# Optimization experiments

Measured on AMD Instinct MI355X. Metric: run time of the kernel, lower is better.

## Reference

```python
import jax, jax.numpy as jnp
import numpy as np

B, A, N, FIN, H, HEADS, OUT = 32, 64, 121, 12, 128, 4, 256
NL = 2          # transformer encoder layers
LEVELS = 4      # complete ternary tree: N = (3**(LEVELS+1)-1)//2 = 121
EPS = 1e-5


def setup_inputs() -> dict:
    key = jax.random.key(0)
    ks = jax.random.split(key, 10)
    s = 0.02
    # adjacency: complete ternary tree, local node indices, rows [parent, child, branch]
    child = np.arange(1, N)
    parent = (child - 1) // 3
    branch = (child - 1) % 3
    adj = np.stack([parent, child, branch], -1).astype(np.int32)  # (N-1, 3)
    adjacency = jnp.asarray(np.broadcast_to(adj, (B, A, N - 1, 3)).copy())
    perm = jax.random.permutation(ks[0], N)  # torch.randperm(n_nodes) equivalent
    forest = jax.random.normal(ks[1], (B, A, N, FIN), jnp.float32)
    p = lambda k, shape: s * jax.random.normal(k, shape, jnp.float32)
    return dict(
        forest=forest, adjacency=adjacency, perm=perm,
        w_in=p(ks[2], (H, FIN)), b_in=jnp.zeros((H,), jnp.float32),
        qkv_w=p(ks[3], (NL, 3 * H, H)), qkv_b=jnp.zeros((NL, 3 * H), jnp.float32),
        proj_w=p(ks[4], (NL, H, H)), proj_b=jnp.zeros((NL, H), jnp.float32),
        ff1_w=p(ks[5], (NL, H, H)), ff1_b=jnp.zeros((NL, H), jnp.float32),
        ff2_w=p(ks[6], (NL, H, H)), ff2_b=jnp.zeros((NL, H), jnp.float32),
        ln1_g=jnp.ones((NL, H), jnp.float32), ln1_b=jnp.zeros((NL, H), jnp.float32),
        ln2_g=jnp.ones((NL, H), jnp.float32), ln2_b=jnp.zeros((NL, H), jnp.float32),
        w_out=p(ks[7], (OUT, N * H)), b_out=jnp.zeros((OUT,), jnp.float32),
        lnf_g=jnp.ones((OUT,), jnp.float32), lnf_b=jnp.zeros((OUT,), jnp.float32))


def _ln(x, g, b):
    m = x.mean(-1, keepdims=True)
    v = ((x - m) ** 2).mean(-1, keepdims=True)  # biased var, as torch LayerNorm
    return (x - m) * jax.lax.rsqrt(v + EPS) * g + b


def _tree_pe(adjacency):
    """Level-parallel tree positional encoding: pe[child] = pe[parent] with
    bit (depth*3 + branch) set to 1 (depth 0 = first level below root)."""
    parent = adjacency[..., 0]
    branch = adjacency[..., 2]
    pe = jnp.zeros((B, A, N, H), jnp.float32)
    for l in range(1, LEVELS + 1):
        s0 = (3 ** l - 1) // 2          # first node index at level l
        e0 = (3 ** (l + 1) - 1) // 2    # one past last node at level l
        pa = parent[..., s0 - 1:e0 - 1]             # (B, A, n_l) parent local idx
        br = branch[..., s0 - 1:e0 - 1]             # (B, A, n_l) branch 0/1/2
        ppe = jnp.take_along_axis(pe, pa[..., None], axis=2)  # gather parent PE
        bits = jax.nn.one_hot((l - 1) * 3 + br, H, dtype=jnp.float32)
        pe = pe.at[:, :, s0:e0, :].set(ppe + bits)
    return pe


def _mha(x, wqkv, bqkv, wo, bo):
    S = x.shape[0]
    hd = H // HEADS
    qkv = x @ wqkv.T + bqkv
    q, k, v = [t.reshape(S, N, HEADS, hd) for t in jnp.split(qkv, 3, axis=-1)]
    logits = jnp.einsum('bqhd,bkhd->bhqk', q, k) / float(np.sqrt(hd))
    o = jnp.einsum('bhqk,bkhd->bqhd', jax.nn.softmax(logits, -1), v)
    return o.reshape(S, N, H) @ wo.T + bo


def _forward(forest, adjacency, perm, w_in, b_in, qkv_w, qkv_b, proj_w, proj_b,
             ff1_w, ff1_b, ff2_w, ff2_b, ln1_g, ln1_b, ln2_g, ln2_b,
             w_out, b_out, lnf_g, lnf_b):
    x = forest @ w_in.T + b_in + _tree_pe(adjacency)        # (B, A, N, H)
    x = x.reshape(B * A, N, H)[:, perm]                      # token shuffle
    for i in range(NL):  # post-norm encoder layers, relu FFN, dropout=0
        x = _ln(x + _mha(x, qkv_w[i], qkv_b[i], proj_w[i], proj_b[i]), ln1_g[i], ln1_b[i])
        h = jnp.maximum(x @ ff1_w[i].T + ff1_b[i], 0.0)
        x = _ln(x + h @ ff2_w[i].T + ff2_b[i], ln2_g[i], ln2_b[i])
    y = x.reshape(B * A, N * H) @ w_out.T + b_out
    return _ln(y.reshape(B, A, OUT), lnf_g, lnf_b)


def reference(forest, adjacency, perm, w_in, b_in, qkv_w, qkv_b, proj_w, proj_b,
              ff1_w, ff1_b, ff2_w, ff2_b, ln1_g, ln1_b, ln2_g, ln2_b,
              w_out, b_out, lnf_g, lnf_b):
    return _forward(forest, adjacency, perm, w_in, b_in, qkv_w, qkv_b, proj_w, proj_b,
                    ff1_w, ff1_b, ff2_w, ff2_b, ln1_g, ln1_b, ln2_g, ln2_b,
                    w_out, b_out, lnf_g, lnf_b)
```

## Files before the change

kernel.cpp:

```cpp
#include <hip/hip_runtime.h>


typedef unsigned short u16;
typedef __attribute__((ext_vector_type(8))) short bf16x8;
typedef __attribute__((ext_vector_type(4))) float f32x4;
typedef __attribute__((ext_vector_type(4))) unsigned int u32x4;
typedef __attribute__((ext_vector_type(2))) unsigned int u32x2;

#define NTOK 121
#define HD 128
#define S_TOT 2048
#define EPSF 1e-5f

__device__ inline u16 f2bf(float f) {
  unsigned u = __float_as_uint(f);
  return (u16)((u + 0x7FFFu + ((u >> 16) & 1u)) >> 16);
}
__device__ inline float bf2f(u16 h) { return __uint_as_float(((unsigned)h) << 16); }
__device__ inline float bfu32lo(unsigned u) { return __uint_as_float(u << 16); }
__device__ inline float bfu32hi(unsigned u) { return __uint_as_float(u & 0xffff0000u); }

__device__ inline f32x4 mfma16(bf16x8 a, bf16x8 b, f32x4 c) {
  return __builtin_amdgcn_mfma_f32_16x16x32_bf16(a, b, c, 0, 0, 0);
}

__device__ inline unsigned cvt_pk_bf16(float lo, float hi) {
  unsigned r;
  asm("v_cvt_pk_bf16_f32 %0, %1, %2" : "=v"(r) : "v"(lo), "v"(hi));
  return r;
}

__device__ inline f32x4 vmax4(f32x4 a, f32x4 b) {
  f32x4 r;
  r[0] = fmaxf(a[0], b[0]); r[1] = fmaxf(a[1], b[1]);
  r[2] = fmaxf(a[2], b[2]); r[3] = fmaxf(a[3], b[3]);
  return r;
}

__device__ inline void stage16(const void* g, void* l) {
  __builtin_amdgcn_global_load_lds((__attribute__((address_space(1))) void*)g,
                                   (__attribute__((address_space(3))) void*)l,
                                   16, 0, 0);
}

__device__ inline void quad_repack(unsigned pkA, unsigned pkB, int quad,
                                   unsigned& mlo, unsigned& mhi) {
  unsigned y = (quad < 2) ? pkA : pkB;
  unsigned z = (quad < 2) ? pkB : pkA;
  unsigned a16 = (unsigned)__shfl_xor((int)y, 16);
  unsigned a32 = (unsigned)__shfl_xor((int)z, 32);
  unsigned a48 = (unsigned)__shfl_xor((int)z, 48);
  mlo = (quad == 0) ? y   : (quad == 1) ? a48 : (quad == 2) ? a32 : a16;
  mhi = (quad == 0) ? a16 : (quad == 1) ? a32 : (quad == 2) ? a48 : y;
}

__global__ __launch_bounds__(256) void convw_kernel(
    const float* __restrict__ qkvw, const float* __restrict__ projw,
    const float* __restrict__ ff1w, const float* __restrict__ ff2w,
    const float* __restrict__ wout, u16* __restrict__ dst) {
  int i = blockIdx.x * 256 + threadIdx.x;
  float v;
  if (i < 98304) v = qkvw[i];
  else if (i < 131072) v = projw[i - 98304];
  else if (i < 163840) v = ff1w[i - 131072];
  else if (i < 196608) v = ff2w[i - 163840];
  else v = wout[i - 196608];
  dst[i] = f2bf(v);
}

__global__ __launch_bounds__(256) void inproj_kernel(
    const float* __restrict__ forest, const int* __restrict__ adj,
    const int* __restrict__ perm, const float* __restrict__ WIN,
    const float* __restrict__ BIN, u16* __restrict__ X) {
  __shared__ float wf[128 * 12];
  __shared__ float fr[121 * 12];
  __shared__ float pe[121 * 12];
  __shared__ int pm[121];
  int s = blockIdx.x, tid = threadIdx.x;
  const float* fg = forest + (size_t)s * (NTOK * 12);
  const int* ag = adj + (size_t)s * (120 * 3);
  for (int i = tid; i < 128 * 12; i += 256) wf[i] = WIN[i];
  for (int i = tid; i < 121 * 12; i += 256) { fr[i] = fg[i]; pe[i] = 0.f; }
  if (tid < 121) pm[tid] = perm[tid];
  __syncthreads();
  if (tid > 0 && tid < 121) {
    int n = tid;
    int l = (n <= 3) ? 1 : (n <= 12) ? 2 : (n <= 39) ? 3 : 4;
    int cur = n;
    while (cur > 0) {
      int par = ag[(cur - 1) * 3];
      int br = ag[(cur - 1) * 3 + 2];
      pe[n * 12 + (l - 1) * 3 + br] = 1.f;
      cur = par; l--;
    }
  }
  __syncthreads();
  int h = tid & 127;
  for (int base = 0; base < 121; base += 2) {
    int i = base + (tid >> 7);
    if (i < 121) {
      int node = pm[i];
      float v = BIN[h];
#pragma unroll
      for (int k = 0; k < 12; ++k) v += fr[node * 12 + k] * wf[h * 12 + k];
      if (h < 12) v += pe[node * 12 + h];
      X[(size_t)s * (NTOK * HD) + i * HD + h] = f2bf(v);
    }
  }
}

__global__ __launch_bounds__(256, 2) void attn_kernel(
    const u16* __restrict__ X, u16* __restrict__ O,
    const u16* __restrict__ WQKV, const float* __restrict__ QKVB, int layer) {
  __shared__ u16 lds[16384];
  __shared__ u16 xl[15872];
  int tid = threadIdx.x;
  int wave = tid >> 6, lane = tid & 63, l16 = lane & 15, quad = lane >> 4;
  int seq = blockIdx.x >> 1;
  int head = ((blockIdx.x & 1) << 1) | (wave >> 1);
  int half = wave & 1;
  int hs = wave >> 1;
  u16* Kh = lds + hs * 4096;
  u16* Vh = lds + 8192 + hs * 4096;
  const u16* Xs = X + (size_t)seq * (NTOK * HD);
  const f32x4 fz = {0.f, 0.f, 0.f, 0.f};
  const int wbase = layer * 384 + head * 32;
  const u16* WQ = WQKV + (size_t)wbase * HD;
  const u16* WK = WQKV + (size_t)(wbase + 128) * HD;
  const u16* WV = WQKV + (size_t)(wbase + 256) * HD;

  {
    const char* Xb = (const char*)Xs;
#pragma unroll
    for (int j = 0; j < 8; ++j) {
      int i = wave * 8 + j;
      if (i < 31) {
        int n = i * 64 + lane;
        int r = n >> 4, c = n & 15;
        int rc = r > 120 ? 120 : r;
        stage16(Xb + rc * 256 + ((c ^ (r & 7)) << 4), (void*)(xl + i * 512));
      }
    }
  }
  bf16x8 wqf[2][4], wkf[2][4], wvf[2][4];
#pragma unroll
  for (int nt = 0; nt < 2; ++nt)
#pragma unroll
    for (int k = 0; k < 4; ++k) {
      size_t off = (size_t)(nt * 16 + l16) * HD + k * 32 + quad * 8;
      wqf[nt][k] = *(const bf16x8*)(WQ + off);
      wkf[nt][k] = *(const bf16x8*)(WK + off);
      wvf[nt][k] = *(const bf16x8*)(WV + off);
    }
  float kb2[2], vb2[2];
#pragma unroll
  for (int nt = 0; nt < 2; ++nt) {
    kb2[nt] = QKVB[wbase + 128 + nt * 16 + l16];
    vb2[nt] = QKVB[wbase + 256 + nt * 16 + l16];
  }
  const float scl = 0.17677669529663687f * 1.4426950408889634f;
  float qbias[2][4];
#pragma unroll
  for (int nt = 0; nt < 2; ++nt)
#pragma unroll
    for (int r = 0; r < 4; ++r)
      qbias[nt][r] = QKVB[wbase + nt * 16 + quad * 4 + r];
  asm volatile("s_waitcnt vmcnt(0)" ::: "memory");
  __syncthreads();

#pragma unroll 1
  for (int mt = 0; mt < 4; ++mt) {
    int tb = half * 64 + mt * 16;
    int arow = tb + l16; if (arow > 120) arow = 120;
    bf16x8 a[4];
#pragma unroll
    for (int k = 0; k < 4; ++k)
      a[k] = *(const bf16x8*)(xl + arow * 128 + (((k * 4 + quad) ^ (arow & 7)) << 3));
#pragma unroll
    for (int nt = 0; nt < 2; ++nt) {
      f32x4 kacc = fz, vacc = fz;
      __builtin_amdgcn_s_setprio(1);
#pragma unroll
      for (int k = 0; k < 4; ++k) {
        kacc = mfma16(a[k], wkf[nt][k], kacc);
        vacc = mfma16(a[k], wvf[nt][k], vacc);
      }
      __builtin_amdgcn_s_setprio(0);
      int d = nt * 16 + l16;
      int kc = nt * 2 + (l16 >> 3);
#pragma unroll
      for (int r = 0; r < 4; ++r) {
        int t = tb + quad * 4 + r;
        Kh[t * 32 + ((kc ^ (t & 3)) << 3) + (l16 & 7)] = f2bf(kacc[r] + kb2[nt]);
      }
      float vv[4];
#pragma unroll
      for (int r = 0; r < 4; ++r) {
        int t = tb + quad * 4 + r;
        vv[r] = (t < NTOK) ? (vacc[r] + vb2[nt]) : 0.f;
      }
      u32x2 vp = { cvt_pk_bf16(vv[0], vv[1]), cvt_pk_bf16(vv[2], vv[3]) };
      *(u32x2*)(Vh + d * 128 + ((((tb >> 3) + (quad >> 1)) ^ l16) << 3) + (quad & 1) * 4) = vp;
    }
  }
  __syncthreads();

#pragma unroll 1
  for (int qmt = 0; qmt < 4; ++qmt) {
    int qb = (half * 4 + qmt) * 16;
    int qrow = qb + l16;
    int qrowc = qrow > 120 ? 120 : qrow;
    bf16x8 xb[4];
#pragma unroll
    for (int k = 0; k < 4; ++k)
      xb[k] = *(const bf16x8*)(xl + qrowc * 128 + (((k * 4 + quad) ^ (qrowc & 7)) << 3));
    f32x4 qv[2];
    __builtin_amdgcn_s_setprio(1);
#pragma unroll
    for (int nt = 0; nt < 2; ++nt) {
      f32x4 acc = fz;
#pragma unroll
      for (int k = 0; k < 4; ++k) acc = mfma16(wqf[nt][k], xb[k], acc);
      qv[nt] = acc;
    }
    __builtin_amdgcn_s_setprio(0);
    unsigned qpk[2][2];
#pragma unroll
    for (int nt = 0; nt < 2; ++nt)
#pragma unroll
      for (int r2 = 0; r2 < 2; ++r2)
        qpk[nt][r2] = cvt_pk_bf16((qv[nt][2 * r2] + qbias[nt][2 * r2]) * scl,
                                  (qv[nt][2 * r2 + 1] + qbias[nt][2 * r2 + 1]) * scl);
    u32x4 qu;
#pragma unroll
    for (int r2 = 0; r2 < 2; ++r2) {
      unsigned mlo, mhi;
      quad_repack(qpk[0][r2], qpk[1][r2], quad, mlo, mhi);
      qu[r2] = mlo; qu[2 + r2] = mhi;
    }
    bf16x8 qfrag = __builtin_bit_cast(bf16x8, qu);
    f32x4 lg[8];
    __builtin_amdgcn_s_setprio(1);
#pragma unroll
    for (int nt = 0; nt < 8; ++nt) {
      bf16x8 ka = *(const bf16x8*)(Kh + (nt * 16 + l16) * 32 + ((quad ^ (l16 & 3)) << 3));
      lg[nt] = mfma16(ka, qfrag, fz);
    }
    __builtin_amdgcn_s_setprio(0);
    f32x4 t0 = vmax4(vmax4(lg[0], lg[1]), vmax4(lg[2], lg[3]));
    f32x4 t1 = vmax4(vmax4(lg[4], lg[5]), vmax4(lg[6], lg[7]));
    f32x4 tm = vmax4(t0, t1);
    float mx = fmaxf(fmaxf(tm[0], tm[1]), fmaxf(tm[2], tm[3]));
    mx = fmaxf(mx, __shfl_xor(mx, 16));
    mx = fmaxf(mx, __shfl_xor(mx, 32));
#pragma unroll
    for (int nt = 0; nt < 8; ++nt)
#pragma unroll
      for (int r = 0; r < 4; ++r) {
        float ev = __builtin_amdgcn_exp2f(lg[nt][r] - mx);
        if (nt == 7 && (quad * 4 + r > 8)) ev = 0.f;
        lg[nt][r] = ev;
      }
    f32x4 s4 = (lg[0] + lg[1]) + (lg[2] + lg[3]) + ((lg[4] + lg[5]) + (lg[6] + lg[7]));
    float sum = (s4[0] + s4[1]) + (s4[2] + s4[3]);
    sum += __shfl_xor(sum, 16);
    sum += __shfl_xor(sum, 32);
    float rinv = __builtin_amdgcn_rcpf(sum);
    unsigned pk[8][2];
#pragma unroll
    for (int nt = 0; nt < 8; ++nt)
#pragma unroll
      for (int r2 = 0; r2 < 2; ++r2)
        pk[nt][r2] = cvt_pk_bf16(lg[nt][2 * r2], lg[nt][2 * r2 + 1]);
    f32x4 oacc[2] = {fz, fz};
#pragma unroll
    for (int s = 0; s < 4; ++s) {
      u32x4 pu;
#pragma unroll
      for (int r2 = 0; r2 < 2; ++r2) {
        unsigned mlo, mhi;
        quad_repack(pk[2 * s][r2], pk[2 * s + 1][r2], quad, mlo, mhi);
        pu[r2] = mlo; pu[2 + r2] = mhi;
      }
      bf16x8 pfrag = __builtin_bit_cast(bf16x8, pu);
      __builtin_amdgcn_s_setprio(1);
#pragma unroll
      for (int mt = 0; mt < 2; ++mt) {
        bf16x8 va = *(const bf16x8*)(Vh + (mt * 16 + l16) * 128 + (((s * 4 + quad) ^ l16) << 3));
        oacc[mt] = mfma16(va, pfrag, oacc[mt]);
      }
      __builtin_amdgcn_s_setprio(0);
    }
    if (qrow < NTOK) {
      u16* Op = O + (size_t)seq * (NTOK * HD) + (size_t)qrow * HD + head * 32;
#pragma unroll
      for (int mt = 0; mt < 2; ++mt) {
        u32x2 w = { cvt_pk_bf16(oacc[mt][0] * rinv, oacc[mt][1] * rinv),
                    cvt_pk_bf16(oacc[mt][2] * rinv, oacc[mt][3] * rinv) };
        *(u32x2*)(Op + mt * 16 + quad * 4) = w;
      }
    }
  }
}

__global__ __launch_bounds__(256, 2) void blockln_kernel(
    u16* __restrict__ X, const u16* __restrict__ O,
    const u16* __restrict__ WP, const float* __restrict__ PB,
    const u16* __restrict__ W1, const float* __restrict__ B1,
    const u16* __restrict__ W2, const float* __restrict__ B2,
    const float* __restrict__ G1, const float* __restrict__ Bt1,
    const float* __restrict__ G2, const float* __restrict__ Bt2, int layer) {
  __shared__ u16 as_[128 * 128];
  __shared__ u16 xr[128 * 128];
  int r0 = blockIdx.x * 128, tid = threadIdx.x;
  int wave = tid >> 6, lane = tid & 63, l16 = lane & 15, quad = lane >> 4;
  const f32x4 fz = {0.f, 0.f, 0.f, 0.f};
  const int Lb = layer * 128;

  {
    const char* Ob = (const char*)(O + (size_t)r0 * HD);
    const char* Xb = (const char*)(X + (size_t)r0 * HD);
#pragma unroll
    for (int j = 0; j < 8; ++j) {
      int n = wave * 512 + j * 64 + lane;
      int r = n >> 4, c = n & 15;
      int gsrc = r * 256 + ((c ^ (r & 7)) << 4);
      stage16(Ob + gsrc, (void*)(as_ + (wave * 512 + j * 64) * 8));
      stage16(Xb + gsrc, (void*)(xr + (wave * 512 + j * 64) * 8));
    }
  }
  asm volatile("s_waitcnt vmcnt(0)" ::: "memory");
  __syncthreads();

  int tok0 = wave * 32 + l16;
  int tok1 = wave * 32 + 16 + l16;

  bf16x8 ofrag[2][4];
#pragma unroll
  for (int k = 0; k < 4; ++k) {
    ofrag[0][k] = *(const bf16x8*)(as_ + tok0 * 128 + (((k * 4 + quad) ^ (tok0 & 7)) << 3));
    ofrag[1][k] = *(const bf16x8*)(as_ + tok1 * 128 + (((k * 4 + quad) ^ (tok1 & 7)) << 3));
  }

  f32x4 acc[8][2];
#pragma unroll
  for (int nt = 0; nt < 8; ++nt) {
    bf16x8 wf[4];
#pragma unroll
    for (int k = 0; k < 4; ++k)
      wf[k] = *(const bf16x8*)(WP + ((size_t)(Lb + nt * 16 + l16)) * HD + k * 32 + quad * 8);
    acc[nt][0] = fz; acc[nt][1] = fz;
    __builtin_amdgcn_s_setprio(1);
#pragma unroll
    for (int k = 0; k < 4; ++k) {
      acc[nt][0] = mfma16(wf[k], ofrag[0][k], acc[nt][0]);
      acc[nt][1] = mfma16(wf[k], ofrag[1][k], acc[nt][1]);
    }
    __builtin_amdgcn_s_setprio(0);
  }

  unsigned pk1[2][8][2];
#pragma unroll
  for (int mt = 0; mt < 2; ++mt) {
    int tok = (mt == 0) ? tok0 : tok1;
    f32x4 v[8];
    float sum = 0.f, ssq = 0.f;
#pragma unroll
    for (int nt = 0; nt < 8; ++nt) {
      float4 pb4 = *(const float4*)(PB + Lb + nt * 16 + quad * 4);
      int chunk = (nt * 2 + (quad >> 1)) ^ (tok & 7);
      u32x2 xw = *(const u32x2*)(xr + tok * 128 + (chunk << 3) + (quad & 1) * 4);
      v[nt][0] = acc[nt][mt][0] + pb4.x + bfu32lo(xw[0]);
      v[nt][1] = acc[nt][mt][1] + pb4.y + bfu32hi(xw[0]);
      v[nt][2] = acc[nt][mt][2] + pb4.z + bfu32lo(xw[1]);
      v[nt][3] = acc[nt][mt][3] + pb4.w + bfu32hi(xw[1]);
#pragma unroll
      for (int r = 0; r < 4; ++r) { sum += v[nt][r]; ssq += v[nt][r] * v[nt][r]; }
    }
    sum += __shfl_xor(sum, 16); sum += __shfl_xor(sum, 32);
    ssq += __shfl_xor(ssq, 16); ssq += __shfl_xor(ssq, 32);
    float mean = sum * (1.f / 128.f);
    float var = ssq * (1.f / 128.f) - mean * mean;
    float rstd = rsqrtf(var + EPSF);
#pragma unroll
    for (int nt = 0; nt < 8; ++nt) {
      float4 g4 = *(const float4*)(G1 + Lb + nt * 16 + quad * 4);
      float4 b4 = *(const float4*)(Bt1 + Lb + nt * 16 + quad * 4);
      float o0 = (v[nt][0] - mean) * rstd * g4.x + b4.x;
      float o1 = (v[nt][1] - mean) * rstd * g4.y + b4.y;
      float o2 = (v[nt][2] - mean) * rstd * g4.z + b4.z;
      float o3 = (v[nt][3] - mean) * rstd * g4.w + b4.w;
      pk1[mt][nt][0] = cvt_pk_bf16(o0, o1);
      pk1[mt][nt][1] = cvt_pk_bf16(o2, o3);
    }
  }

  bf16x8 pfrag[2][4];
#pragma unroll
  for (int mt = 0; mt < 2; ++mt)
#pragma unroll
    for (int s = 0; s < 4; ++s) {
      u32x4 pu;
#pragma unroll
      for (int r2 = 0; r2 < 2; ++r2) {
        unsigned mlo, mhi;
        quad_repack(pk1[mt][2 * s][r2], pk1[mt][2 * s + 1][r2], quad, mlo, mhi);
        pu[r2] = mlo; pu[2 + r2] = mhi;
      }
      pfrag[mt][s] = __builtin_bit_cast(bf16x8, pu);
    }
  f32x4 acc2[8][2];
#pragma unroll
  for (int nt = 0; nt < 8; ++nt) {
    bf16x8 wf[4];
#pragma unroll
    for (int k = 0; k < 4; ++k)
      wf[k] = *(const bf16x8*)(W1 + ((size_t)(Lb + nt * 16 + l16)) * HD + k * 32 + quad * 8);
    acc2[nt][0] = fz; acc2[nt][1] = fz;
    __builtin_amdgcn_s_setprio(1);
#pragma unroll
    for (int k = 0; k < 4; ++k) {
      acc2[nt][0] = mfma16(wf[k], pfrag[0][k], acc2[nt][0]);
      acc2[nt][1] = mfma16(wf[k], pfrag[1][k], acc2[nt][1]);
    }
    __builtin_amdgcn_s_setprio(0);
  }

  unsigned pk2[2][8][2];
#pragma unroll
  for (int nt = 0; nt < 8; ++nt) {
    float4 b14 = *(const float4*)(B1 + Lb + nt * 16 + quad * 4);
#pragma unroll
    for (int mt = 0; mt < 2; ++mt) {
      float h0 = fmaxf(acc2[nt][mt][0] + b14.x, 0.f);
      float h1 = fmaxf(acc2[nt][mt][1] + b14.y, 0.f);
      float h2 = fmaxf(acc2[nt][mt][2] + b14.z, 0.f);
      float h3 = fmaxf(acc2[nt][mt][3] + b14.w, 0.f);
      pk2[mt][nt][0] = cvt_pk_bf16(h0, h1);
      pk2[mt][nt][1] = cvt_pk_bf16(h2, h3);
    }
  }
  bf16x8 hfrag[2][4];
#pragma unroll
  for (int mt = 0; mt < 2; ++mt)
#pragma unroll
    for (int s = 0; s < 4; ++s) {
      u32x4 pu;
#pragma unroll
      for (int r2 = 0; r2 < 2; ++r2) {
        unsigned mlo, mhi;
        quad_repack(pk2[mt][2 * s][r2], pk2[mt][2 * s + 1][r2], quad, mlo, mhi);
        pu[r2] = mlo; pu[2 + r2] = mhi;
      }
      hfrag[mt][s] = __builtin_bit_cast(bf16x8, pu);
    }

  f32x4 acc3[8][2];
#pragma unroll
  for (int nt = 0; nt < 8; ++nt) {
    bf16x8 wf[4];
#pragma unroll
    for (int k = 0; k < 4; ++k)
      wf[k] = *(const bf16x8*)(W2 + ((size_t)(Lb + nt * 16 + l16)) * HD + k * 32 + quad * 8);
    acc3[nt][0] = fz; acc3[nt][1] = fz;
    __builtin_amdgcn_s_setprio(1);
#pragma unroll
    for (int k = 0; k < 4; ++k) {
      acc3[nt][0] = mfma16(wf[k], hfrag[0][k], acc3[nt][0]);
      acc3[nt][1] = mfma16(wf[k], hfrag[1][k], acc3[nt][1]);
    }
    __builtin_amdgcn_s_setprio(0);
  }

#pragma unroll
  for (int mt = 0; mt < 2; ++mt) {
    int tok = (mt == 0) ? tok0 : tok1;
    f32x4 v[8];
    float sum = 0.f, ssq = 0.f;
#pragma unroll
    for (int nt = 0; nt < 8; ++nt) {
      float4 b24 = *(const float4*)(B2 + Lb + nt * 16 + quad * 4);
      v[nt][0] = acc3[nt][mt][0] + b24.x + bfu32lo(pk1[mt][nt][0]);
      v[nt][1] = acc3[nt][mt][1] + b24.y + bfu32hi(pk1[mt][nt][0]);
      v[nt][2] = acc3[nt][mt][2] + b24.z + bfu32lo(pk1[mt][nt][1]);
      v[nt][3] = acc3[nt][mt][3] + b24.w + bfu32hi(pk1[mt][nt][1]);
#pragma unroll
      for (int r = 0; r < 4; ++r) { sum += v[nt][r]; ssq += v[nt][r] * v[nt][r]; }
    }
    sum += __shfl_xor(sum, 16); sum += __shfl_xor(sum, 32);
    ssq += __shfl_xor(ssq, 16); ssq += __shfl_xor(ssq, 32);
    float mean = sum * (1.f / 128.f);
    float var = ssq * (1.f / 128.f) - mean * mean;
    float rstd = rsqrtf(var + EPSF);
    u16* Xp = X + (size_t)(r0 + tok) * HD;
#pragma unroll
    for (int nt = 0; nt < 8; ++nt) {
      float4 g4 = *(const float4*)(G2 + Lb + nt * 16 + quad * 4);
      float4 b4 = *(const float4*)(Bt2 + Lb + nt * 16 + quad * 4);
      float o0 = (v[nt][0] - mean) * rstd * g4.x + b4.x;
      float o1 = (v[nt][1] - mean) * rstd * g4.y + b4.y;
      float o2 = (v[nt][2] - mean) * rstd * g4.z + b4.z;
      float o3 = (v[nt][3] - mean) * rstd * g4.w + b4.w;
      u32x2 w = { cvt_pk_bf16(o0, o1), cvt_pk_bf16(o2, o3) };
      *(u32x2*)(Xp + nt * 16 + quad * 4) = w;
    }
  }
}

__global__ __launch_bounds__(256, 2) void outgemm_kernel(
    const u16* __restrict__ X, const u16* __restrict__ WO, float* __restrict__ PART) {
  __shared__ u16 as_[64 * 136];
  int mtile = blockIdx.x, j = blockIdx.y;
  int tid = threadIdx.x, wave = tid >> 6, lane = tid & 63, l16 = lane & 15, quad = lane >> 4;
  int s0 = mtile * 64;
  int k0 = (j * 484) / 16, k1 = ((j + 1) * 484) / 16;
  const f32x4 fz = {0.f, 0.f, 0.f, 0.f};
  f32x4 acc[4][4];
  for (int a = 0; a < 4; ++a) for (int b = 0; b < 4; ++b) acc[a][b] = fz;
  for (int kb = k0; kb < k1; kb += 4) {
    int nst = (k1 - kb < 4) ? (k1 - kb) : 4;
    __syncthreads();
    int chunks = 64 * 4 * nst;
    for (int c = tid; c < chunks; c += 256) {
      int row = c / (4 * nst), g = c % (4 * nst);
      *(uint4*)(as_ + row * 136 + g * 8) =
          *(const uint4*)(X + (size_t)(s0 + row) * 15488 + kb * 32 + g * 8);
    }
    __syncthreads();
    for (int kk = 0; kk < nst; ++kk) {
      bf16x8 af[4];
#pragma unroll
      for (int mt = 0; mt < 4; ++mt)
        af[mt] = *(const bf16x8*)(as_ + (mt * 16 + l16) * 136 + kk * 32 + quad * 8);
#pragma unroll
      for (int n = 0; n < 4; ++n) {
        int nt = wave * 4 + n;
        bf16x8 bf = *(const bf16x8*)(WO + (size_t)(nt * 16 + l16) * 15488 +
                                     (size_t)(kb + kk) * 32 + quad * 8);
#pragma unroll
        for (int mt = 0; mt < 4; ++mt) acc[mt][n] = mfma16(af[mt], bf, acc[mt][n]);
      }
    }
  }
  for (int mt = 0; mt < 4; ++mt)
    for (int n = 0; n < 4; ++n) {
      int nt = wave * 4 + n;
#pragma unroll
      for (int r = 0; r < 4; ++r) {
        int row = s0 + mt * 16 + quad * 4 + r;
        PART[((size_t)j * 2048 + row) * 256 + nt * 16 + l16] = acc[mt][n][r];
      }
    }
}

__global__ __launch_bounds__(256) void lnf_kernel(
    const float* __restrict__ PART, const float* __restrict__ BO,
    const float* __restrict__ G, const float* __restrict__ Bt, float* __restrict__ OUT) {
  int s = blockIdx.x * 4 + (threadIdx.x >> 6);
  int lane = threadIdx.x & 63;
  float v[4], sum = 0.f, ssq = 0.f;
#pragma unroll
  for (int i = 0; i < 4; ++i) {
    int c = lane + i * 64;
    float t = BO[c];
    for (int jj = 0; jj < 16; ++jj) t += PART[((size_t)jj * 2048 + s) * 256 + c];
    v[i] = t; sum += t; ssq += t * t;
  }
  for (int m = 1; m <= 32; m <<= 1) { sum += __shfl_xor(sum, m, 64); ssq += __shfl_xor(ssq, m, 64); }
  float mean = sum * (1.f / 256.f);
  float var = ssq * (1.f / 256.f) - mean * mean;
  float rstd = rsqrtf(var + EPSF);
#pragma unroll
  for (int i = 0; i < 4; ++i) {
    int c = lane + i * 64;
    OUT[(size_t)s * 256 + c] = (v[i] - mean) * rstd * G[c] + Bt[c];
  }
}

extern "C" void kernel_launch(void* const* d_in, const int* in_sizes, int n_in,
                              void* d_out, int out_size, void* d_ws, size_t ws_size,
                              hipStream_t stream) {
  const float* forest = (const float*)d_in[0];
  const int* adj      = (const int*)d_in[1];
  const int* perm     = (const int*)d_in[2];
  const float* w_in   = (const float*)d_in[3];
  const float* b_in   = (const float*)d_in[4];
  const float* qkv_w  = (const float*)d_in[5];
  const float* qkv_b  = (const float*)d_in[6];
  const float* proj_w = (const float*)d_in[7];
  const float* proj_b = (const float*)d_in[8];
  const float* ff1_w  = (const float*)d_in[9];
  const float* ff1_b  = (const float*)d_in[10];
  const float* ff2_w  = (const float*)d_in[11];
  const float* ff2_b  = (const float*)d_in[12];
  const float* ln1_g  = (const float*)d_in[13];
  const float* ln1_b  = (const float*)d_in[14];
  const float* ln2_g  = (const float*)d_in[15];
  const float* ln2_b  = (const float*)d_in[16];
  const float* w_out  = (const float*)d_in[17];
  const float* b_out  = (const float*)d_in[18];
  const float* lnf_g  = (const float*)d_in[19];
  const float* lnf_b  = (const float*)d_in[20];

  char* ws = (char*)d_ws;
  u16* WB = (u16*)ws;
  u16* X  = (u16*)(ws + 8323072);
  u16* O  = (u16*)(ws + 8323072 + 63438848);
  float* PART = (float*)(ws + 8323072 + 2 * (size_t)63438848);

  u16* WQKV  = WB;
  u16* WPROJ = WB + 98304;
  u16* WFF1  = WB + 131072;
  u16* WFF2  = WB + 163840;
  u16* WOUT  = WB + 196608;

  convw_kernel<<<16256, 256, 0, stream>>>(qkv_w, proj_w, ff1_w, ff2_w, w_out, WB);
  inproj_kernel<<<2048, 256, 0, stream>>>(forest, adj, perm, w_in, b_in, X);
  for (int layer = 0; layer < 2; ++layer) {
    attn_kernel<<<4096, 256, 0, stream>>>(X, O, WQKV, qkv_b, layer);
    blockln_kernel<<<1936, 256, 0, stream>>>(X, O, WPROJ, proj_b, WFF1, ff1_b,
                                             WFF2, ff2_b, ln1_g, ln1_b, ln2_g, ln2_b, layer);
  }
  outgemm_kernel<<<dim3(32, 16), 256, 0, stream>>>(X, WOUT, PART);
  lnf_kernel<<<512, 256, 0, stream>>>(PART, b_out, lnf_g, lnf_b, (float*)d_out);
}
```

Before: 689.5 us.

## Split blockln work by output channels so each wave keeps its weights in registers

The fused proj+LN+FFN+LN kernel now gives each wave 32 output channels across all 128 tokens, not 32 tokens across all channels. Each wave loads its slice of the three weight matrices into registers once, overlapped with the activation staging, instead of streaming the full weight matrices from global memory per wave. Because LayerNorm now needs row statistics spread across waves, partial sums go through a small shared buffer. Intermediate activations move through LDS with extra barriers, replacing the register quad repacking.

```diff
diff --git a/kernel.cpp b/kernel.cpp
--- a/kernel.cpp
+++ b/kernel.cpp
@@ -312,10 +312,13 @@
     const float* __restrict__ G2, const float* __restrict__ Bt2, int layer) {
   __shared__ u16 as_[128 * 128];
   __shared__ u16 xr[128 * 128];
+  __shared__ float part[1024];
   int r0 = blockIdx.x * 128, tid = threadIdx.x;
   int wave = tid >> 6, lane = tid & 63, l16 = lane & 15, quad = lane >> 4;
   const f32x4 fz = {0.f, 0.f, 0.f, 0.f};
   const int Lb = layer * 128;
+  const int ch0 = wave * 32;
+  const int ch8b = wave * 4 + (quad >> 1);
 
   {
     const char* Ob = (const char*)(O + (size_t)r0 * HD);
@@ -329,180 +332,159 @@
       stage16(Xb + gsrc, (void*)(xr + (wave * 512 + j * 64) * 8));
     }
   }
+  bf16x8 wpf[2][4], w1f[2][4], w2f[2][4];
+#pragma unroll
+  for (int g = 0; g < 2; ++g)
+#pragma unroll
+    for (int k = 0; k < 4; ++k) {
+      size_t off = (size_t)(Lb + ch0 + g * 16 + l16) * HD + k * 32 + quad * 8;
+      wpf[g][k] = *(const bf16x8*)(WP + off);
+      w1f[g][k] = *(const bf16x8*)(W1 + off);
+      w2f[g][k] = *(const bf16x8*)(W2 + off);
+    }
   asm volatile("s_waitcnt vmcnt(0)" ::: "memory");
   __syncthreads();
 
-  int tok0 = wave * 32 + l16;
-  int tok1 = wave * 32 + 16 + l16;
-
-  bf16x8 ofrag[2][4];
-#pragma unroll
-  for (int k = 0; k < 4; ++k) {
-    ofrag[0][k] = *(const bf16x8*)(as_ + tok0 * 128 + (((k * 4 + quad) ^ (tok0 & 7)) << 3));
-    ofrag[1][k] = *(const bf16x8*)(as_ + tok1 * 128 + (((k * 4 + quad) ^ (tok1 & 7)) << 3));
-  }
-
-  f32x4 acc[8][2];
-#pragma unroll
-  for (int nt = 0; nt < 8; ++nt) {
-    bf16x8 wf[4];
+  f32x4 acc[2][8];
+#pragma unroll
+  for (int mt = 0; mt < 8; ++mt) {
+    int tok = mt * 16 + l16;
+    bf16x8 of[4];
 #pragma unroll
     for (int k = 0; k < 4; ++k)
-      wf[k] = *(const bf16x8*)(WP + ((size_t)(Lb + nt * 16 + l16)) * HD + k * 32 + quad * 8);
-    acc[nt][0] = fz; acc[nt][1] = fz;
+      of[k] = *(const bf16x8*)(as_ + tok * 128 + (((k * 4 + quad) ^ (tok & 7)) << 3));
     __builtin_amdgcn_s_setprio(1);
 #pragma unroll
-    for (int k = 0; k < 4; ++k) {
-      acc[nt][0] = mfma16(wf[k], ofrag[0][k], acc[nt][0]);
-      acc[nt][1] = mfma16(wf[k], ofrag[1][k], acc[nt][1]);
+    for (int g = 0; g < 2; ++g) {
+      f32x4 a = fz;
+#pragma unroll
+      for (int k = 0; k < 4; ++k) a = mfma16(wpf[g][k], of[k], a);
+      acc[g][mt] = a;
     }
     __builtin_amdgcn_s_setprio(0);
-  }
-
-  unsigned pk1[2][8][2];
-#pragma unroll
-  for (int mt = 0; mt < 2; ++mt) {
-    int tok = (mt == 0) ? tok0 : tok1;
-    f32x4 v[8];
     float sum = 0.f, ssq = 0.f;
 #pragma unroll
-    for (int nt = 0; nt < 8; ++nt) {
-      float4 pb4 = *(const float4*)(PB + Lb + nt * 16 + quad * 4);
-      int chunk = (nt * 2 + (quad >> 1)) ^ (tok & 7);
-      u32x2 xw = *(const u32x2*)(xr + tok * 128 + (chunk << 3) + (quad & 1) * 4);
-      v[nt][0] = acc[nt][mt][0] + pb4.x + bfu32lo(xw[0]);
-      v[nt][1] = acc[nt][mt][1] + pb4.y + bfu32hi(xw[0]);
-      v[nt][2] = acc[nt][mt][2] + pb4.z + bfu32lo(xw[1]);
-      v[nt][3] = acc[nt][mt][3] + pb4.w + bfu32hi(xw[1]);
-#pragma unroll
-      for (int r = 0; r < 4; ++r) { sum += v[nt][r]; ssq += v[nt][r] * v[nt][r]; }
-    }
-    sum += __shfl_xor(sum, 16); sum += __shfl_xor(sum, 32);
-    ssq += __shfl_xor(ssq, 16); ssq += __shfl_xor(ssq, 32);
+    for (int g = 0; g < 2; ++g) {
+      float4 pb4 = *(const float4*)(PB + Lb + ch0 + g * 16 + quad * 4);
+      int sl = (ch8b + g * 2) ^ (tok & 7);
+      u32x2 xw = *(const u32x2*)(xr + tok * 128 + (sl << 3) + (quad & 1) * 4);
+      acc[g][mt][0] += pb4.x + bfu32lo(xw[0]);
+      acc[g][mt][1] += pb4.y + bfu32hi(xw[0]);
+      acc[g][mt][2] += pb4.z + bfu32lo(xw[1]);
+      acc[g][mt][3] += pb4.w + bfu32hi(xw[1]);
+#pragma unroll
+      for (int r = 0; r < 4; ++r) { sum += acc[g][mt][r]; ssq += acc[g][mt][r] * acc[g][mt][r]; }
+    }
+    sum += __shfl_xor(sum, 16); ssq += __shfl_xor(ssq, 16);
+    sum += __shfl_xor(sum, 32); ssq += __shfl_xor(ssq, 32);
+    if (quad == 0) *(float2*)(part + ((mt * 4 + wave) * 16 + l16) * 2) = make_float2(sum, ssq);
+  }
+  __syncthreads();
+
+#pragma unroll
+  for (int mt = 0; mt < 8; ++mt) {
+    int tok = mt * 16 + l16;
+    float sum = 0.f, ssq = 0.f;
+#pragma unroll
+    for (int ww = 0; ww < 4; ++ww) {
+      float2 p = *(const float2*)(part + ((mt * 4 + ww) * 16 + l16) * 2);
+      sum += p.x; ssq += p.y;
+    }
     float mean = sum * (1.f / 128.f);
-    float var = ssq * (1.f / 128.f) - mean * mean;
-    float rstd = rsqrtf(var + EPSF);
-#pragma unroll
-    for (int nt = 0; nt < 8; ++nt) {
-      float4 g4 = *(const float4*)(G1 + Lb + nt * 16 + quad * 4);
-      float4 b4 = *(const float4*)(Bt1 + Lb + nt * 16 + quad * 4);
-      float o0 = (v[nt][0] - mean) * rstd * g4.x + b4.x;
-      float o1 = (v[nt][1] - mean) * rstd * g4.y + b4.y;
-      float o2 = (v[nt][2] - mean) * rstd * g4.z + b4.z;
-      float o3 = (v[nt][3] - mean) * rstd * g4.w + b4.w;
-      pk1[mt][nt][0] = cvt_pk_bf16(o0, o1);
-      pk1[mt][nt][1] = cvt_pk_bf16(o2, o3);
-    }
-  }
-
-  bf16x8 pfrag[2][4];
-#pragma unroll
-  for (int mt = 0; mt < 2; ++mt)
-#pragma unroll
-    for (int s = 0; s < 4; ++s) {
-      u32x4 pu;
-#pragma unroll
-      for (int r2 = 0; r2 < 2; ++r2) {
-        unsigned mlo, mhi;
-        quad_repack(pk1[mt][2 * s][r2], pk1[mt][2 * s + 1][r2], quad, mlo, mhi);
-        pu[r2] = mlo; pu[2 + r2] = mhi;
-      }
-      pfrag[mt][s] = __builtin_bit_cast(bf16x8, pu);
-    }
-  f32x4 acc2[8][2];
-#pragma unroll
-  for (int nt = 0; nt < 8; ++nt) {
-    bf16x8 wf[4];
+    float rstd = rsqrtf(ssq * (1.f / 128.f) - mean * mean + EPSF);
+#pragma unroll
+    for (int g = 0; g < 2; ++g) {
+      float4 g4 = *(const float4*)(G1 + Lb + ch0 + g * 16 + quad * 4);
+      float4 b4 = *(const float4*)(Bt1 + Lb + ch0 + g * 16 + quad * 4);
+      u32x2 wv = { cvt_pk_bf16((acc[g][mt][0] - mean) * rstd * g4.x + b4.x,
+                               (acc[g][mt][1] - mean) * rstd * g4.y + b4.y),
+                   cvt_pk_bf16((acc[g][mt][2] - mean) * rstd * g4.z + b4.z,
+                               (acc[g][mt][3] - mean) * rstd * g4.w + b4.w) };
+      int sl = (ch8b + g * 2) ^ (tok & 7);
+      *(u32x2*)(as_ + tok * 128 + (sl << 3) + (quad & 1) * 4) = wv;
+    }
+  }
+  __syncthreads();
+
+#pragma unroll
+  for (int mt = 0; mt < 8; ++mt) {
+    int tok = mt * 16 + l16;
+    bf16x8 af[4];
 #pragma unroll
     for (int k = 0; k < 4; ++k)
-      wf[k] = *(const bf16x8*)(W1 + ((size_t)(Lb + nt * 16 + l16)) * HD + k * 32 + quad * 8);
-    acc2[nt][0] = fz; acc2[nt][1] = fz;
+      af[k] = *(const bf16x8*)(as_ + tok * 128 + (((k * 4 + quad) ^ (tok & 7)) << 3));
     __builtin_amdgcn_s_setprio(1);
 #pragma unroll
-    for (int k = 0; k < 4; ++k) {
-      acc2[nt][0] = mfma16(wf[k], pfrag[0][k], acc2[nt][0]);
-      acc2[nt][1] = mfma16(wf[k], pfrag[1][k], acc2[nt][1]);
+    for (int g = 0; g < 2; ++g) {
+      f32x4 a = fz;
+#pragma unroll
+      for (int k = 0; k < 4; ++k) a = mfma16(w1f[g][k], af[k], a);
+      float4 b14 = *(const float4*)(B1 + Lb + ch0 + g * 16 + quad * 4);
+      u32x2 wv = { cvt_pk_bf16(fmaxf(a[0] + b14.x, 0.f), fmaxf(a[1] + b14.y, 0.f)),
+                   cvt_pk_bf16(fmaxf(a[2] + b14.z, 0.f), fmaxf(a[3] + b14.w, 0.f)) };
+      int sl = (ch8b + g * 2) ^ (tok & 7);
+      *(u32x2*)(xr + tok * 128 + (sl << 3) + (quad & 1) * 4) = wv;
     }
     __builtin_amdgcn_s_setprio(0);
   }
-
-  unsigned pk2[2][8][2];
-#pragma unroll
-  for (int nt = 0; nt < 8; ++nt) {
-    float4 b14 = *(const float4*)(B1 + Lb + nt * 16 + quad * 4);
-#pragma unroll
-    for (int mt = 0; mt < 2; ++mt) {
-      float h0 = fmaxf(acc2[nt][mt][0] + b14.x, 0.f);
-      float h1 = fmaxf(acc2[nt][mt][1] + b14.y, 0.f);
-      float h2 = fmaxf(acc2[nt][mt][2] + b14.z, 0.f);
-      float h3 = fmaxf(acc2[nt][mt][3] + b14.w, 0.f);
-      pk2[mt][nt][0] = cvt_pk_bf16(h0, h1);
-      pk2[mt][nt][1] = cvt_pk_bf16(h2, h3);
-    }
-  }
-  bf16x8 hfrag[2][4];
-#pragma unroll
-  for (int mt = 0; mt < 2; ++mt)
-#pragma unroll
-    for (int s = 0; s < 4; ++s) {
-      u32x4 pu;
-#pragma unroll
-      for (int r2 = 0; r2 < 2; ++r2) {
-        unsigned mlo, mhi;
-        quad_repack(pk2[mt][2 * s][r2], pk2[mt][2 * s + 1][r2], quad, mlo, mhi);
-        pu[r2] = mlo; pu[2 + r2] = mhi;
-      }
-      hfrag[mt][s] = __builtin_bit_cast(bf16x8, pu);
-    }
-
-  f32x4 acc3[8][2];
-#pragma unroll
-  for (int nt = 0; nt < 8; ++nt) {
-    bf16x8 wf[4];
+  __syncthreads();
+
+#pragma unroll
+  for (int mt = 0; mt < 8; ++mt) {
+    int tok = mt * 16 + l16;
+    bf16x8 hf[4];
 #pragma unroll
     for (int k = 0; k < 4; ++k)
-      wf[k] = *(const bf16x8*)(W2 + ((size_t)(Lb + nt * 16 + l16)) * HD + k * 32 + quad * 8);
-    acc3[nt][0] = fz; acc3[nt][1] = fz;
+      hf[k] = *(const bf16x8*)(xr + tok * 128 + (((k * 4 + quad) ^ (tok & 7)) << 3));
     __builtin_amdgcn_s_setprio(1);
 #pragma unroll
-    for (int k = 0; k < 4; ++k) {
-      acc3[nt][0] = mfma16(wf[k], hfrag[0][k], acc3[nt][0]);
-      acc3[nt][1] = mfma16(wf[k], hfrag[1][k], acc3[nt][1]);
+    for (int g = 0; g < 2; ++g) {
+      f32x4 a = fz;
+#pragma unroll
+      for (int k = 0; k < 4; ++k) a = mfma16(w2f[g][k], hf[k], a);
+      acc[g][mt] = a;
     }
     __builtin_amdgcn_s_setprio(0);
-  }
-
-#pragma unroll
-  for (int mt = 0; mt < 2; ++mt) {
-    int tok = (mt == 0) ? tok0 : tok1;
-    f32x4 v[8];
     float sum = 0.f, ssq = 0.f;
 #pragma unroll
-    for (int nt = 0; nt < 8; ++nt) {
-      float4 b24 = *(const float4*)(B2 + Lb + nt * 16 + quad * 4);
-      v[nt][0] = acc3[nt][mt][0] + b24.x + bfu32lo(pk1[mt][nt][0]);
-      v[nt][1] = acc3[nt][mt][1] + b24.y + bfu32hi(pk1[mt][nt][0]);
-      v[nt][2] = acc3[nt][mt][2] + b24.z + bfu32lo(pk1[mt][nt][1]);
-      v[nt][3] = acc3[nt][mt][3] + b24.w + bfu32hi(pk1[mt][nt][1]);
-#pragma unroll
-      for (int r = 0; r < 4; ++r) { sum += v[nt][r]; ssq += v[nt][r] * v[nt][r]; }
-    }
-    sum += __shfl_xor(sum, 16); sum += __shfl_xor(sum, 32);
-    ssq += __shfl_xor(ssq, 16); ssq += __shfl_xor(ssq, 32);
+    for (int g = 0; g < 2; ++g) {
+      float4 b24 = *(const float4*)(B2 + Lb + ch0 + g * 16 + quad * 4);
+      int sl = (ch8b + g * 2) ^ (tok & 7);
+      u32x2 lw = *(const u32x2*)(as_ + tok * 128 + (sl << 3) + (quad & 1) * 4);
+      acc[g][mt][0] += b24.x + bfu32lo(lw[0]);
+      acc[g][mt][1] += b24.y + bfu32hi(lw[0]);
+      acc[g][mt][2] += b24.z + bfu32lo(lw[1]);
+      acc[g][mt][3] += b24.w + bfu32hi(lw[1]);
+#pragma unroll
+      for (int r = 0; r < 4; ++r) { sum += acc[g][mt][r]; ssq += acc[g][mt][r] * acc[g][mt][r]; }
+    }
+    sum += __shfl_xor(sum, 16); ssq += __shfl_xor(ssq, 16);
+    sum += __shfl_xor(sum, 32); ssq += __shfl_xor(ssq, 32);
+    if (quad == 0) *(float2*)(part + ((mt * 4 + wave) * 16 + l16) * 2) = make_float2(sum, ssq);
+  }
+  __syncthreads();
+
+#pragma unroll
+  for (int mt = 0; mt < 8; ++mt) {
+    int tok = mt * 16 + l16;
+    float sum = 0.f, ssq = 0.f;
+#pragma unroll
+    for (int ww = 0; ww < 4; ++ww) {
+      float2 p = *(const float2*)(part + ((mt * 4 + ww) * 16 + l16) * 2);
+      sum += p.x; ssq += p.y;
+    }
     float mean = sum * (1.f / 128.f);
-    float var = ssq * (1.f / 128.f) - mean * mean;
-    float rstd = rsqrtf(var + EPSF);
-    u16* Xp = X + (size_t)(r0 + tok) * HD;
-#pragma unroll
-    for (int nt = 0; nt < 8; ++nt) {
-      float4 g4 = *(const float4*)(G2 + Lb + nt * 16 + quad * 4);
-      float4 b4 = *(const float4*)(Bt2 + Lb + nt * 16 + quad * 4);
-      float o0 = (v[nt][0] - mean) * rstd * g4.x + b4.x;
-      float o1 = (v[nt][1] - mean) * rstd * g4.y + b4.y;
-      float o2 = (v[nt][2] - mean) * rstd * g4.z + b4.z;
-      float o3 = (v[nt][3] - mean) * rstd * g4.w + b4.w;
-      u32x2 w = { cvt_pk_bf16(o0, o1), cvt_pk_bf16(o2, o3) };
-      *(u32x2*)(Xp + nt * 16 + quad * 4) = w;
+    float rstd = rsqrtf(ssq * (1.f / 128.f) - mean * mean + EPSF);
+    u16* Xp = X + (size_t)(r0 + tok) * HD + ch0;
+#pragma unroll
+    for (int g = 0; g < 2; ++g) {
+      float4 g4 = *(const float4*)(G2 + Lb + ch0 + g * 16 + quad * 4);
+      float4 b4 = *(const float4*)(Bt2 + Lb + ch0 + g * 16 + quad * 4);
+      u32x2 wv = { cvt_pk_bf16((acc[g][mt][0] - mean) * rstd * g4.x + b4.x,
+                               (acc[g][mt][1] - mean) * rstd * g4.y + b4.y),
+                   cvt_pk_bf16((acc[g][mt][2] - mean) * rstd * g4.z + b4.z,
+                               (acc[g][mt][3] - mean) * rstd * g4.w + b4.w) };
+      *(u32x2*)(Xp + g * 16 + quad * 4) = wv;
     }
   }
 }
```

New measurement: 593.8 us. 13.9% less time.
